# Kernel tuning notes

Hardware: AMD Instinct MI355X
Metric: run time of the kernel (lower is better)

Reference implementation:

```python
import jax, jax.numpy as jnp
import numpy as np

NUM_HEADS = 4
NUM_GROUPS = 8
EPS = 1e-5


def setup_inputs() -> dict:
    key = jax.random.key(0)
    ks = jax.random.split(key, 7)
    B, C, T, H, W = 2, 256, 16, 16, 16
    return {
        "x": jax.random.normal(ks[0], (B, C, T, H, W), dtype=jnp.float32),
        "norm_w": jax.random.normal(ks[1], (C,), dtype=jnp.float32),
        "norm_b": jax.random.normal(ks[2], (C,), dtype=jnp.float32),
        "qkv_w": jax.random.normal(ks[3], (3 * C, C), dtype=jnp.float32) * (C ** -0.5),
        "qkv_b": jax.random.normal(ks[4], (3 * C,), dtype=jnp.float32) * 0.02,
        "proj_w": jax.random.normal(ks[5], (C, C), dtype=jnp.float32) * (C ** -0.5),
        "proj_b": jax.random.normal(ks[6], (C,), dtype=jnp.float32) * 0.02,
    }


def reference(x, norm_w, norm_b, qkv_w, qkv_b, proj_w, proj_b):
    B, C, T, H, W = x.shape
    N = T * H * W
    hd = C // NUM_HEADS  # head dim

    # GroupNorm(8, C): stats over (C//G, T, H, W) per group
    xg = x.reshape(B, NUM_GROUPS, -1)
    mean = jnp.mean(xg, axis=-1, keepdims=True)
    var = jnp.var(xg, axis=-1, keepdims=True)
    xn = ((xg - mean) * jax.lax.rsqrt(var + EPS)).reshape(B, C, N)
    xn = xn * norm_w[None, :, None] + norm_b[None, :, None]

    # 1x1 conv3d qkv == per-token linear: (B, 3C, N)
    qkv = jnp.einsum('oc,bcn->bon', qkv_w, xn) + qkv_b[None, :, None]
    # reshape(B,3,heads,hd,N).permute(1,0,2,4,3) -> (3, B, heads, N, hd)
    qkv = qkv.reshape(B, 3, NUM_HEADS, hd, N).transpose(1, 0, 2, 4, 3)
    q, k, v = qkv[0], qkv[1], qkv[2]

    scale = hd ** -0.5
    scores = jnp.einsum('bhnd,bhmd->bhnm', q, k) * scale  # (B, heads, N, N)
    attn = jax.nn.softmax(scores, axis=-1)
    h = jnp.einsum('bhnm,bhmd->bhnd', attn, v)  # (B, heads, N, hd)

    # permute(0,1,3,2).reshape(B, C, T, H, W) -> channels-first tokens
    h = h.transpose(0, 1, 3, 2).reshape(B, C, N)
    out = jnp.einsum('oc,bcn->bon', proj_w, h) + proj_b[None, :, None]
    return out.reshape(B, C, T, H, W) + x
```

## Files before the change

### kernel.cpp

```cpp
#include <hip/hip_runtime.h>
#include <math.h>

#define B_DIM 2
#define C_DIM 256
#define N_TOK 4096
#define HEADS 4
#define HD 64
#define GROUPS 8
#define CPG (C_DIM / GROUPS)
#define EPS 1e-5f
#define PSB 72
#define QK_SCALE 0.180336880f
#define KSPLIT 4
#define NKT (N_TOK / 64)
#define QBLK 256

typedef __bf16 bf16x8 __attribute__((ext_vector_type(8)));
typedef float  f32x4  __attribute__((ext_vector_type(4)));
typedef unsigned short u16x4v __attribute__((ext_vector_type(4)));
typedef unsigned short u16x8v __attribute__((ext_vector_type(8)));

__device__ __forceinline__ unsigned short f2bf(float f) {
    return __builtin_bit_cast(unsigned short, (__bf16)f);
}
__device__ __forceinline__ float bf2f(unsigned short u) {
    return (float)__builtin_bit_cast(__bf16, u);
}
__device__ __forceinline__ float exp2_fast(float x) { return __builtin_amdgcn_exp2f(x); }

__device__ __forceinline__ void gload16(const unsigned short* g, unsigned short* l) {
    __builtin_amdgcn_global_load_lds(
        (const __attribute__((address_space(1))) unsigned int*)g,
        (__attribute__((address_space(3))) unsigned int*)l, 16, 0, 0);
}

__device__ __forceinline__ int kperm(int r) {
    return (r & 0x23) | ((r & 0x0C) << 1) | ((r & 0x10) >> 2);
}

__global__ __launch_bounds__(256) void gn_part_kernel(const float* __restrict__ x,
                                                      float* __restrict__ partials) {
    const int bg = blockIdx.x >> 6, ch = blockIdx.x & 63;
    const float4* p = (const float4*)(x + (size_t)bg * CPG * N_TOK) + ch * 512;
    float s = 0.f, ss = 0.f;
#pragma unroll
    for (int r = 0; r < 2; ++r) {
        float4 v = p[threadIdx.x + (r << 8)];
        s  += v.x + v.y + v.z + v.w;
        ss += v.x * v.x + v.y * v.y + v.z * v.z + v.w * v.w;
    }
#pragma unroll
    for (int off = 32; off > 0; off >>= 1) {
        s  += __shfl_down(s, off);
        ss += __shfl_down(ss, off);
    }
    __shared__ float ls[4], lss[4];
    const int lane = threadIdx.x & 63, wid = threadIdx.x >> 6;
    if (lane == 0) { ls[wid] = s; lss[wid] = ss; }
    __syncthreads();
    if (threadIdx.x == 0) {
        partials[blockIdx.x * 2 + 0] = ls[0] + ls[1] + ls[2] + ls[3];
        partials[blockIdx.x * 2 + 1] = lss[0] + lss[1] + lss[2] + lss[3];
    }
}

__global__ __launch_bounds__(256) void qkv_gemm_kernel(
    const float* __restrict__ x, const float* __restrict__ partials,
    const float* __restrict__ norm_w, const float* __restrict__ norm_b,
    const float* __restrict__ qkv_w, const float* __restrict__ qkv_b,
    unsigned short* __restrict__ qkvb) {
    __shared__ unsigned short Ws[64][PSB];
    __shared__ unsigned short Xt[64][PSB];
    __shared__ float stat_s[GROUPS][2];
    const int n0 = blockIdx.x * 64;
    const int o0 = blockIdx.y * 64;
    const int b  = blockIdx.z;
    const int tid = threadIdx.x;
    const int lane = tid & 63, w = tid >> 6;
    const int lo = lane & 15, hi = lane >> 4;

    {
        const int g = tid >> 5, sub = tid & 31;
        const float* pp = partials + (((size_t)b * GROUPS + g) * 64 + sub * 2) * 2;
        float4 v = *(const float4*)pp;
        float s = v.x + v.z, ss = v.y + v.w;
#pragma unroll
        for (int off = 16; off > 0; off >>= 1) {
            s  += __shfl_down(s, off, 32);
            ss += __shfl_down(ss, off, 32);
        }
        if (sub == 0) {
            const float inv = 1.f / (float)(CPG * N_TOK);
            float mean = s * inv;
            float var  = ss * inv - mean * mean;
            stat_s[g][0] = mean;
            stat_s[g][1] = rsqrtf(var + EPS);
        }
        __syncthreads();
    }

    f32x4 acc[4] = {};
    for (int k0 = 0; k0 < C_DIM; k0 += 64) {
#pragma unroll
        for (int r = 0; r < 4; ++r) {
            int idx = tid + (r << 8);
            int row = idx >> 4, col4 = (idx & 15) << 2;
            float4 wv = *(const float4*)(qkv_w + (size_t)(o0 + row) * C_DIM + k0 + col4);
            u16x4v o;
            o[0] = f2bf(wv.x); o[1] = f2bf(wv.y); o[2] = f2bf(wv.z); o[3] = f2bf(wv.w);
            *(u16x4v*)&Ws[row][col4] = o;
        }
#pragma unroll
        for (int r = 0; r < 4; ++r) {
            int idx = tid + (r << 8);
            int crow = idx >> 4, col4 = (idx & 15) << 2;
            int c = k0 + crow;
            int g = c >> 5;
            float ww = norm_w[c] * stat_s[g][1];
            float bb = norm_b[c] - stat_s[g][0] * ww;
            float4 v = *(const float4*)(x + ((size_t)b * C_DIM + c) * N_TOK + n0 + col4);
            Xt[col4 + 0][crow] = f2bf(v.x * ww + bb);
            Xt[col4 + 1][crow] = f2bf(v.y * ww + bb);
            Xt[col4 + 2][crow] = f2bf(v.z * ww + bb);
            Xt[col4 + 3][crow] = f2bf(v.w * ww + bb);
        }
        __syncthreads();
#pragma unroll
        for (int ck = 0; ck < 2; ++ck) {
            bf16x8 aw = *(const bf16x8*)&Ws[w * 16 + lo][ck * 32 + hi * 8];
#pragma unroll
            for (int nb = 0; nb < 4; ++nb)
                acc[nb] = __builtin_amdgcn_mfma_f32_16x16x32_bf16(
                    aw, *(const bf16x8*)&Xt[nb * 16 + lo][ck * 32 + hi * 8], acc[nb], 0, 0, 0);
        }
        __syncthreads();
    }

    const int sidx = o0 >> 8;
    const int head = (o0 >> 6) & 3;
    const int od = w * 16 + hi * 4;
    float bias[4];
#pragma unroll
    for (int i = 0; i < 4; ++i) bias[i] = qkv_b[o0 + od + i];
    const size_t plane = (size_t)N_TOK * HD;

    if (sidx < 2) {
        const float sc = (sidx == 0) ? QK_SCALE : 1.0f;
        unsigned short* base = qkvb + ((size_t)(sidx * B_DIM + b) * HEADS + head) * plane;
#pragma unroll
        for (int nb = 0; nb < 4; ++nb) {
            int n = n0 + nb * 16 + lo;
            u16x4v o;
#pragma unroll
            for (int i = 0; i < 4; ++i) o[i] = f2bf((acc[nb][i] + bias[i]) * sc);
            *(u16x4v*)(base + (size_t)n * HD + od) = o;
        }
    } else {
        unsigned short* base = qkvb + (size_t)2 * B_DIM * HEADS * plane
                             + ((size_t)b * HEADS + head) * plane;
#pragma unroll
        for (int nb = 0; nb < 4; ++nb)
#pragma unroll
            for (int i = 0; i < 4; ++i)
                base[(size_t)(od + i) * N_TOK + n0 + nb * 16 + lo] = f2bf(acc[nb][i] + bias[i]);
    }
}

__global__ __launch_bounds__(512, 4) void attn_kernel(const unsigned short* __restrict__ qkvb,
                                                      unsigned short* __restrict__ obuf,
                                                      float* __restrict__ rbuf) {
    const int bh = blockIdx.x & 7;
    const int ks = (blockIdx.x >> 3) & 3;
    const int q0 = (blockIdx.x >> 5) * QBLK;
    const size_t plane = (size_t)N_TOK * HD;
    const unsigned short* Qg  = qkvb + (size_t)bh * plane;
    const unsigned short* Kg  = qkvb + (size_t)(B_DIM * HEADS + bh) * plane;
    const unsigned short* Vtg = qkvb + (size_t)2 * B_DIM * HEADS * plane + (size_t)bh * plane;

    __shared__ unsigned short Ks[2][64][64];
    __shared__ unsigned short Vt[2][64][64];

    const int tid  = threadIdx.x;
    const int lane = tid & 63;
    const int wid  = tid >> 6;
    const int lo   = lane & 15;
    const int hi   = lane >> 4;

    bf16x8 qf[2][2];
#pragma unroll
    for (int f = 0; f < 2; ++f)
#pragma unroll
        for (int c = 0; c < 2; ++c)
            qf[f][c] = *(const bf16x8*)(Qg + (size_t)(q0 + wid * 32 + f * 16 + lo) * HD
                                            + c * 32 + hi * 8);

    const int srow = tid >> 3, sblk = tid & 7;
    const int c16s = (sblk ^ (srow & 7)) * 8;
    const int krow = kperm(srow);
    int rcol[2];
#pragma unroll
    for (int c = 0; c < 2; ++c) rcol[c] = (((c * 4 + hi) ^ (lo & 7)) << 3);

#define STAGE_KV(bufi, kbase)                                                          \
    do {                                                                               \
        gload16(Kg + (size_t)((kbase) + krow) * HD + c16s, &Ks[bufi][wid * 8][0]);     \
        gload16(Vtg + (size_t)srow * N_TOK + (kbase) + c16s, &Vt[bufi][wid * 8][0]);   \
    } while (0)

    const int kt0 = ks * (NKT / KSPLIT), ktE = kt0 + NKT / KSPLIT;

    f32x4 acc[2][4] = {};
    float m[2] = {-1e30f, -1e30f}, l[2] = {0.f, 0.f};

    STAGE_KV(0, kt0 * 64);
    __syncthreads();

    for (int kt = kt0; kt < ktE; ++kt) {
        const int cur = kt & 1;
        if (kt + 1 < ktE) STAGE_KV(cur ^ 1, (kt + 1) * 64);

        f32x4 s4[2][4] = {};
        __builtin_amdgcn_s_setprio(1);
#pragma unroll
        for (int kb = 0; kb < 4; ++kb)
#pragma unroll
            for (int c = 0; c < 2; ++c) {
                bf16x8 kf = *(const bf16x8*)&Ks[cur][kb * 16 + lo][rcol[c]];
                s4[0][kb] = __builtin_amdgcn_mfma_f32_16x16x32_bf16(kf, qf[0][c], s4[0][kb], 0, 0, 0);
                s4[1][kb] = __builtin_amdgcn_mfma_f32_16x16x32_bf16(kf, qf[1][c], s4[1][kb], 0, 0, 0);
            }
        __builtin_amdgcn_s_setprio(0);

        bf16x8 pf[2][2];
#pragma unroll
        for (int f = 0; f < 2; ++f) {
            float r0 = fmaxf(fmaxf(fmaxf(s4[f][0][0], s4[f][0][1]), s4[f][0][2]), s4[f][0][3]);
            float r1 = fmaxf(fmaxf(fmaxf(s4[f][1][0], s4[f][1][1]), s4[f][1][2]), s4[f][1][3]);
            float r2 = fmaxf(fmaxf(fmaxf(s4[f][2][0], s4[f][2][1]), s4[f][2][2]), s4[f][2][3]);
            float r3 = fmaxf(fmaxf(fmaxf(s4[f][3][0], s4[f][3][1]), s4[f][3][2]), s4[f][3][3]);
            float rm = fmaxf(fmaxf(fmaxf(r0, r1), r2), r3);

            if (__any(rm > m[f] + 8.0f)) {
                float rmx = rm;
                rmx = fmaxf(rmx, __shfl_xor(rmx, 16));
                rmx = fmaxf(rmx, __shfl_xor(rmx, 32));
                const float mn = fmaxf(m[f], rmx);
                const float fi = exp2_fast(m[f] - mn);
                m[f] = mn;
                l[f] *= fi;
#pragma unroll
                for (int db = 0; db < 4; ++db)
#pragma unroll
                    for (int i = 0; i < 4; ++i) acc[f][db][i] *= fi;
            }

            float p[4][4];
            float ps = 0.f;
#pragma unroll
            for (int kb = 0; kb < 4; ++kb)
#pragma unroll
                for (int i = 0; i < 4; ++i) {
                    p[kb][i] = exp2_fast(s4[f][kb][i] - m[f]);
                    ps += p[kb][i];
                }
            l[f] += ps;

#pragma unroll
            for (int c = 0; c < 2; ++c)
#pragma unroll
                for (int j = 0; j < 8; ++j) pf[f][c][j] = (__bf16)p[2 * c + (j >> 2)][j & 3];
        }

        __builtin_amdgcn_s_setprio(1);
#pragma unroll
        for (int db = 0; db < 4; ++db)
#pragma unroll
            for (int c = 0; c < 2; ++c) {
                bf16x8 vf = *(const bf16x8*)&Vt[cur][db * 16 + lo][rcol[c]];
                acc[0][db] = __builtin_amdgcn_mfma_f32_16x16x32_bf16(vf, pf[0][c], acc[0][db], 0, 0, 0);
                acc[1][db] = __builtin_amdgcn_mfma_f32_16x16x32_bf16(vf, pf[1][c], acc[1][db], 0, 0, 0);
            }
        __builtin_amdgcn_s_setprio(0);

        __syncthreads();
    }
#undef STAGE_KV

#pragma unroll
    for (int f = 0; f < 2; ++f) {
        float l1 = l[f] + __shfl_xor(l[f], 16);
        float lt = l1 + __shfl_xor(l1, 32);
        const float inv = 1.f / lt;
        const int n = q0 + wid * 32 + f * 16 + lo;
        unsigned short* ob = obuf + ((size_t)(ks * 8 + bh) * N_TOK + n) * HD;
#pragma unroll
        for (int db = 0; db < 4; ++db) {
            u16x4v o;
#pragma unroll
            for (int i = 0; i < 4; ++i) o[i] = f2bf(acc[f][db][i] * inv);
            *(u16x4v*)(ob + db * 16 + hi * 4) = o;
        }
        if (hi == 0)
            rbuf[(size_t)(ks * 8 + bh) * N_TOK + n] = m[f] + __builtin_amdgcn_logf(lt);
    }
}

__global__ __launch_bounds__(256) void proj_kernel(
    const unsigned short* __restrict__ obuf, const float* __restrict__ rbuf,
    const float* __restrict__ proj_w, const float* __restrict__ proj_b,
    const float* __restrict__ x, float* __restrict__ out) {
    __shared__ unsigned short Ws[64][PSB];
    __shared__ unsigned short Hs[64][PSB];
    const int n0 = blockIdx.x * 64;
    const int o0 = blockIdx.y * 64;
    const int b  = blockIdx.z;
    const int tid = threadIdx.x;
    const int lane = tid & 63, w = tid >> 6;
    const int lo = lane & 15, hi = lane >> 4;
    f32x4 acc[4] = {};

    for (int k0 = 0; k0 < C_DIM; k0 += 64) {
#pragma unroll
        for (int r = 0; r < 4; ++r) {
            int idx = tid + (r << 8);
            int row = idx >> 4, col4 = (idx & 15) << 2;
            float4 wv = *(const float4*)(proj_w + (size_t)(o0 + row) * C_DIM + k0 + col4);
            u16x4v o;
            o[0] = f2bf(wv.x); o[1] = f2bf(wv.y); o[2] = f2bf(wv.z); o[3] = f2bf(wv.w);
            *(u16x4v*)&Ws[row][col4] = o;
        }
        {
            const int head = k0 >> 6;
            const int bh = b * HEADS + head;
#pragma unroll
            for (int r = 0; r < 2; ++r) {
                int idx = tid + (r << 8);
                int row = idx >> 3, blk = idx & 7;
                int n = n0 + row;
                float rr[KSPLIT], M = -1e30f;
#pragma unroll
                for (int k = 0; k < KSPLIT; ++k) {
                    rr[k] = rbuf[(size_t)(k * 8 + bh) * N_TOK + n];
                    M = fmaxf(M, rr[k]);
                }
                float wk[KSPLIT], tot = 0.f;
#pragma unroll
                for (int k = 0; k < KSPLIT; ++k) { wk[k] = exp2_fast(rr[k] - M); tot += wk[k]; }
                const float inv = 1.f / tot;
                float a[8] = {};
#pragma unroll
                for (int k = 0; k < KSPLIT; ++k) {
                    u16x8v v = *(const u16x8v*)(obuf
                        + ((size_t)(k * 8 + bh) * N_TOK + n) * HD + blk * 8);
#pragma unroll
                    for (int j = 0; j < 8; ++j) a[j] += wk[k] * bf2f(v[j]);
                }
                u16x8v o;
#pragma unroll
                for (int j = 0; j < 8; ++j) o[j] = f2bf(a[j] * inv);
                *(u16x8v*)&Hs[row][blk * 8] = o;
            }
        }
        __syncthreads();
#pragma unroll
        for (int ck = 0; ck < 2; ++ck) {
            bf16x8 aw = *(const bf16x8*)&Ws[w * 16 + lo][ck * 32 + hi * 8];
#pragma unroll
            for (int nb = 0; nb < 4; ++nb)
                acc[nb] = __builtin_amdgcn_mfma_f32_16x16x32_bf16(
                    aw, *(const bf16x8*)&Hs[nb * 16 + lo][ck * 32 + hi * 8], acc[nb], 0, 0, 0);
        }
        __syncthreads();
    }

#pragma unroll
    for (int nb = 0; nb < 4; ++nb) {
#pragma unroll
        for (int i = 0; i < 4; ++i) {
            int o = o0 + w * 16 + hi * 4 + i;
            size_t addr = ((size_t)b * C_DIM + o) * N_TOK + n0 + nb * 16 + lo;
            out[addr] = acc[nb][i] + proj_b[o] + x[addr];
        }
    }
}

extern "C" void kernel_launch(void* const* d_in, const int* in_sizes, int n_in,
                              void* d_out, int out_size, void* d_ws, size_t ws_size,
                              hipStream_t stream) {
    const float* x      = (const float*)d_in[0];
    const float* norm_w = (const float*)d_in[1];
    const float* norm_b = (const float*)d_in[2];
    const float* qkv_w  = (const float*)d_in[3];
    const float* qkv_b  = (const float*)d_in[4];
    const float* proj_w = (const float*)d_in[5];
    const float* proj_b = (const float*)d_in[6];
    float* out = (float*)d_out;

    float* partials = (float*)d_ws;
    unsigned short* qkvb = (unsigned short*)(partials + 2048);
    unsigned short* obuf = qkvb + (size_t)3 * B_DIM * HEADS * N_TOK * HD;
    float* rbuf = (float*)(obuf + (size_t)KSPLIT * B_DIM * HEADS * N_TOK * HD);

    gn_part_kernel<<<B_DIM * GROUPS * 64, 256, 0, stream>>>(x, partials);
    qkv_gemm_kernel<<<dim3(N_TOK / 64, 3 * C_DIM / 64, B_DIM), 256, 0, stream>>>(
        x, partials, norm_w, norm_b, qkv_w, qkv_b, qkvb);
    attn_kernel<<<(N_TOK / QBLK) * B_DIM * HEADS * KSPLIT, 512, 0, stream>>>(qkvb, obuf, rbuf);
    proj_kernel<<<dim3(N_TOK / 64, C_DIM / 64, B_DIM), 256, 0, stream>>>(
        obuf, rbuf, proj_w, proj_b, x, out);
}
```

Measured before the change: 93.09 us.

## Pre-convert weights to bf16 and split attention combine into separate kernel

The GroupNorm partial-stats kernel now also converts the qkv and proj weights to bf16 into the workspace, so the GEMM kernels can load weight tiles with direct global-to-LDS 16-byte loads into an XOR-swizzled layout instead of converting fp32 in every block. The split-K attention combine moves out of the projection kernel into a new kernel that writes a token-major bf16 activation buffer (reusing the qkv buffer). The projection GEMM then streams both operands via direct LDS loads. This removes redundant weight conversion and the combine work repeated across the four output-channel blocks, at the cost of an extra launch and an extra round trip of the combined activations through memory.

Result: faster. 90.83 us (-2.4%).

```diff
diff --git a/kernel.cpp b/kernel.cpp
--- a/kernel.cpp
+++ b/kernel.cpp
@@ -14,6 +14,8 @@
 #define KSPLIT 4
 #define NKT (N_TOK / 64)
 #define QBLK 256
+#define NQKVW (3 * C_DIM * C_DIM)
+#define NPROJW (C_DIM * C_DIM)
 
 typedef __bf16 bf16x8 __attribute__((ext_vector_type(8)));
 typedef float  f32x4  __attribute__((ext_vector_type(4)));
@@ -39,7 +41,10 @@
 }
 
 __global__ __launch_bounds__(256) void gn_part_kernel(const float* __restrict__ x,
-                                                      float* __restrict__ partials) {
+                                                      const float* __restrict__ qkv_w,
+                                                      const float* __restrict__ proj_w,
+                                                      float* __restrict__ partials,
+                                                      unsigned short* __restrict__ wbf) {
     const int bg = blockIdx.x >> 6, ch = blockIdx.x & 63;
     const float4* p = (const float4*)(x + (size_t)bg * CPG * N_TOK) + ch * 512;
     float s = 0.f, ss = 0.f;
@@ -57,6 +62,11 @@
     __shared__ float ls[4], lss[4];
     const int lane = threadIdx.x & 63, wid = threadIdx.x >> 6;
     if (lane == 0) { ls[wid] = s; lss[wid] = ss; }
+
+    const int widx = blockIdx.x * 256 + threadIdx.x;
+    float wv = (widx < NQKVW) ? qkv_w[widx] : proj_w[widx - NQKVW];
+    wbf[widx] = f2bf(wv);
+
     __syncthreads();
     if (threadIdx.x == 0) {
         partials[blockIdx.x * 2 + 0] = ls[0] + ls[1] + ls[2] + ls[3];
@@ -67,9 +77,9 @@
 __global__ __launch_bounds__(256) void qkv_gemm_kernel(
     const float* __restrict__ x, const float* __restrict__ partials,
     const float* __restrict__ norm_w, const float* __restrict__ norm_b,
-    const float* __restrict__ qkv_w, const float* __restrict__ qkv_b,
+    const unsigned short* __restrict__ wqbf, const float* __restrict__ qkv_b,
     unsigned short* __restrict__ qkvb) {
-    __shared__ unsigned short Ws[64][PSB];
+    __shared__ unsigned short Ws[64][64];
     __shared__ unsigned short Xt[64][PSB];
     __shared__ float stat_s[GROUPS][2];
     const int n0 = blockIdx.x * 64;
@@ -78,6 +88,11 @@
     const int tid = threadIdx.x;
     const int lane = tid & 63, w = tid >> 6;
     const int lo = lane & 15, hi = lane >> 4;
+    const int srow8 = lane >> 3, sblk = lane & 7;
+    const int c16s = (sblk ^ srow8) * 8;
+    int rcol[2];
+#pragma unroll
+    for (int c = 0; c < 2; ++c) rcol[c] = (((c * 4 + hi) ^ (lo & 7)) << 3);
 
     {
         const int g = tid >> 5, sub = tid & 31;
@@ -102,13 +117,9 @@
     f32x4 acc[4] = {};
     for (int k0 = 0; k0 < C_DIM; k0 += 64) {
 #pragma unroll
-        for (int r = 0; r < 4; ++r) {
-            int idx = tid + (r << 8);
-            int row = idx >> 4, col4 = (idx & 15) << 2;
-            float4 wv = *(const float4*)(qkv_w + (size_t)(o0 + row) * C_DIM + k0 + col4);
-            u16x4v o;
-            o[0] = f2bf(wv.x); o[1] = f2bf(wv.y); o[2] = f2bf(wv.z); o[3] = f2bf(wv.w);
-            *(u16x4v*)&Ws[row][col4] = o;
+        for (int i = 0; i < 2; ++i) {
+            int row = i * 32 + w * 8 + srow8;
+            gload16(wqbf + (size_t)(o0 + row) * C_DIM + k0 + c16s, &Ws[i * 32 + w * 8][0]);
         }
 #pragma unroll
         for (int r = 0; r < 4; ++r) {
@@ -127,7 +138,7 @@
         __syncthreads();
 #pragma unroll
         for (int ck = 0; ck < 2; ++ck) {
-            bf16x8 aw = *(const bf16x8*)&Ws[w * 16 + lo][ck * 32 + hi * 8];
+            bf16x8 aw = *(const bf16x8*)&Ws[w * 16 + lo][rcol[ck]];
 #pragma unroll
             for (int nb = 0; nb < 4; ++nb)
                 acc[nb] = __builtin_amdgcn_mfma_f32_16x16x32_bf16(
@@ -305,70 +316,77 @@
     }
 }
 
+__global__ __launch_bounds__(256) void attn_combine_kernel(
+    const unsigned short* __restrict__ obuf, const float* __restrict__ rbuf,
+    unsigned short* __restrict__ hT) {
+    const int idx = blockIdx.x * 256 + threadIdx.x;
+    const int dq  = (idx & 3) * 16;
+    const int bhn = idx >> 2;
+    const int n   = bhn & (N_TOK - 1);
+    const int bh  = bhn >> 12;
+    float r[KSPLIT], M = -1e30f;
+#pragma unroll
+    for (int k = 0; k < KSPLIT; ++k) {
+        r[k] = rbuf[(size_t)(k * 8 + bh) * N_TOK + n];
+        M = fmaxf(M, r[k]);
+    }
+    float w[KSPLIT], tot = 0.f;
+#pragma unroll
+    for (int k = 0; k < KSPLIT; ++k) { w[k] = exp2_fast(r[k] - M); tot += w[k]; }
+    const float inv = 1.f / tot;
+    const int b = bh >> 2, head = bh & 3;
+    unsigned short* dst = hT + ((size_t)b * N_TOK + n) * C_DIM + head * HD + dq;
+#pragma unroll
+    for (int c = 0; c < 2; ++c) {
+        float a[8] = {};
+#pragma unroll
+        for (int k = 0; k < KSPLIT; ++k) {
+            u16x8v v = *(const u16x8v*)(obuf + ((size_t)(k * 8 + bh) * N_TOK + n) * HD + dq + c * 8);
+#pragma unroll
+            for (int j = 0; j < 8; ++j) a[j] += w[k] * bf2f(v[j]);
+        }
+        u16x8v o;
+#pragma unroll
+        for (int j = 0; j < 8; ++j) o[j] = f2bf(a[j] * inv);
+        *(u16x8v*)(dst + c * 8) = o;
+    }
+}
+
 __global__ __launch_bounds__(256) void proj_kernel(
-    const unsigned short* __restrict__ obuf, const float* __restrict__ rbuf,
-    const float* __restrict__ proj_w, const float* __restrict__ proj_b,
-    const float* __restrict__ x, float* __restrict__ out) {
-    __shared__ unsigned short Ws[64][PSB];
-    __shared__ unsigned short Hs[64][PSB];
+    const unsigned short* __restrict__ hT, const unsigned short* __restrict__ wpbf,
+    const float* __restrict__ proj_b, const float* __restrict__ x,
+    float* __restrict__ out) {
+    __shared__ unsigned short Ws[64][64];
+    __shared__ unsigned short Hs[64][64];
     const int n0 = blockIdx.x * 64;
     const int o0 = blockIdx.y * 64;
     const int b  = blockIdx.z;
     const int tid = threadIdx.x;
     const int lane = tid & 63, w = tid >> 6;
     const int lo = lane & 15, hi = lane >> 4;
+    const int srow8 = lane >> 3, sblk = lane & 7;
+    const int c16s = (sblk ^ srow8) * 8;
+    int rcol[2];
+#pragma unroll
+    for (int c = 0; c < 2; ++c) rcol[c] = (((c * 4 + hi) ^ (lo & 7)) << 3);
+
     f32x4 acc[4] = {};
-
     for (int k0 = 0; k0 < C_DIM; k0 += 64) {
 #pragma unroll
-        for (int r = 0; r < 4; ++r) {
-            int idx = tid + (r << 8);
-            int row = idx >> 4, col4 = (idx & 15) << 2;
-            float4 wv = *(const float4*)(proj_w + (size_t)(o0 + row) * C_DIM + k0 + col4);
-            u16x4v o;
-            o[0] = f2bf(wv.x); o[1] = f2bf(wv.y); o[2] = f2bf(wv.z); o[3] = f2bf(wv.w);
-            *(u16x4v*)&Ws[row][col4] = o;
-        }
-        {
-            const int head = k0 >> 6;
-            const int bh = b * HEADS + head;
-#pragma unroll
-            for (int r = 0; r < 2; ++r) {
-                int idx = tid + (r << 8);
-                int row = idx >> 3, blk = idx & 7;
-                int n = n0 + row;
-                float rr[KSPLIT], M = -1e30f;
-#pragma unroll
-                for (int k = 0; k < KSPLIT; ++k) {
-                    rr[k] = rbuf[(size_t)(k * 8 + bh) * N_TOK + n];
-                    M = fmaxf(M, rr[k]);
-                }
-                float wk[KSPLIT], tot = 0.f;
-#pragma unroll
-                for (int k = 0; k < KSPLIT; ++k) { wk[k] = exp2_fast(rr[k] - M); tot += wk[k]; }
-                const float inv = 1.f / tot;
-                float a[8] = {};
-#pragma unroll
-                for (int k = 0; k < KSPLIT; ++k) {
-                    u16x8v v = *(const u16x8v*)(obuf
-                        + ((size_t)(k * 8 + bh) * N_TOK + n) * HD + blk * 8);
-#pragma unroll
-                    for (int j = 0; j < 8; ++j) a[j] += wk[k] * bf2f(v[j]);
-                }
-                u16x8v o;
-#pragma unroll
-                for (int j = 0; j < 8; ++j) o[j] = f2bf(a[j] * inv);
-                *(u16x8v*)&Hs[row][blk * 8] = o;
-            }
+        for (int i = 0; i < 2; ++i) {
+            int row = i * 32 + w * 8 + srow8;
+            gload16(wpbf + (size_t)(o0 + row) * C_DIM + k0 + c16s, &Ws[i * 32 + w * 8][0]);
+            gload16(hT + ((size_t)b * N_TOK + n0 + row) * C_DIM + k0 + c16s,
+                    &Hs[i * 32 + w * 8][0]);
         }
         __syncthreads();
 #pragma unroll
         for (int ck = 0; ck < 2; ++ck) {
-            bf16x8 aw = *(const bf16x8*)&Ws[w * 16 + lo][ck * 32 + hi * 8];
+            bf16x8 aw = *(const bf16x8*)&Ws[w * 16 + lo][rcol[ck]];
 #pragma unroll
             for (int nb = 0; nb < 4; ++nb)
                 acc[nb] = __builtin_amdgcn_mfma_f32_16x16x32_bf16(
-                    aw, *(const bf16x8*)&Hs[nb * 16 + lo][ck * 32 + hi * 8], acc[nb], 0, 0, 0);
+                    aw, *(const bf16x8*)&Hs[nb * 16 + lo][rcol[ck]], acc[nb], 0, 0, 0);
         }
         __syncthreads();
     }
@@ -397,14 +415,19 @@
     float* out = (float*)d_out;
 
     float* partials = (float*)d_ws;
-    unsigned short* qkvb = (unsigned short*)(partials + 2048);
+    unsigned short* wbf = (unsigned short*)(partials + 2048);
+    unsigned short* qkvb = wbf + (NQKVW + NPROJW);
+    unsigned short* hT = qkvb;
     unsigned short* obuf = qkvb + (size_t)3 * B_DIM * HEADS * N_TOK * HD;
     float* rbuf = (float*)(obuf + (size_t)KSPLIT * B_DIM * HEADS * N_TOK * HD);
-
-    gn_part_kernel<<<B_DIM * GROUPS * 64, 256, 0, stream>>>(x, partials);
+    const unsigned short* wqbf = wbf;
+    const unsigned short* wpbf = wbf + NQKVW;
+
+    gn_part_kernel<<<B_DIM * GROUPS * 64, 256, 0, stream>>>(x, qkv_w, proj_w, partials, wbf);
     qkv_gemm_kernel<<<dim3(N_TOK / 64, 3 * C_DIM / 64, B_DIM), 256, 0, stream>>>(
-        x, partials, norm_w, norm_b, qkv_w, qkv_b, qkvb);
+        x, partials, norm_w, norm_b, wqbf, qkv_b, qkvb);
     attn_kernel<<<(N_TOK / QBLK) * B_DIM * HEADS * KSPLIT, 512, 0, stream>>>(qkvb, obuf, rbuf);
+    attn_combine_kernel<<<B_DIM * HEADS * N_TOK * 4 / 256, 256, 0, stream>>>(obuf, rbuf, hT);
     proj_kernel<<<dim3(N_TOK / 64, C_DIM / 64, B_DIM), 256, 0, stream>>>(
-        obuf, rbuf, proj_w, proj_b, x, out);
-}
+        hT, wpbf, proj_b, x, out);
+}
```
